# Optimization experiments

Hardware: AMD Instinct MI355X
Metric: run time of the kernel (lower is better)

The kernel has to match this reference:

```python
import jax, jax.numpy as jnp
import numpy as np

HEADS = 4
NEG_SLOPE = 0.2  # PyG GATConv default


def gat_layer(x, src, dst, W, a_src, a_dst, b):
    """PyG-style GATConv: gather -> per-edge attention -> segment softmax -> scatter.
    x: [N, Fin], W: [Fin, H*C], a_src/a_dst: [H, C], b: [H*C]."""
    N = x.shape[0]
    h = (x @ W).reshape(N, HEADS, -1)                      # [N, H, C]
    alpha_s = jnp.einsum('nhc,hc->nh', h, a_src)           # [N, H]
    alpha_d = jnp.einsum('nhc,hc->nh', h, a_dst)           # [N, H]
    e = jax.nn.leaky_relu(alpha_s[src] + alpha_d[dst], NEG_SLOPE)  # [E, H]
    # segment softmax over incoming edges of each destination node
    m = jax.ops.segment_max(e, dst, num_segments=N)
    m = jnp.where(jnp.isfinite(m), m, 0.0)
    ex = jnp.exp(e - m[dst])
    denom = jax.ops.segment_sum(ex, dst, num_segments=N)
    alpha = ex / (denom[dst] + 1e-16)                      # [E, H]
    msg = h[src] * alpha[:, :, None]                       # [E, H, C]
    out = jax.ops.segment_sum(msg, dst, num_segments=N)    # [N, H, C]
    return out.reshape(N, -1) + b


def setup_inputs() -> dict:
    key = jax.random.key(0)
    ks = jax.random.split(key, 10)
    N, E, FIN, HID, OUT = 50000, 800000, 128, 128, 128
    hd1, hd2 = HID // HEADS, OUT // HEADS
    x = jax.random.normal(ks[0], (N, FIN), dtype=jnp.float32)
    edge_index = jax.random.randint(ks[1], (2, E), 0, N, dtype=jnp.int32)
    s1 = 1.0 / np.sqrt(FIN)
    s2 = 1.0 / np.sqrt(HID)
    return {
        'x_sub': x,
        'edge_index_sub': edge_index,
        'W1': jax.random.normal(ks[2], (FIN, HEADS * hd1), dtype=jnp.float32) * s1,
        'a_src1': jax.random.normal(ks[3], (HEADS, hd1), dtype=jnp.float32) * 0.1,
        'a_dst1': jax.random.normal(ks[4], (HEADS, hd1), dtype=jnp.float32) * 0.1,
        'b1': jnp.zeros((HEADS * hd1,), dtype=jnp.float32),
        'W2': jax.random.normal(ks[5], (HID, HEADS * hd2), dtype=jnp.float32) * s2,
        'a_src2': jax.random.normal(ks[6], (HEADS, hd2), dtype=jnp.float32) * 0.1,
        'a_dst2': jax.random.normal(ks[7], (HEADS, hd2), dtype=jnp.float32) * 0.1,
        'b2': jnp.zeros((HEADS * hd2,), dtype=jnp.float32),
    }


def reference(x_sub, edge_index_sub, W1, a_src1, a_dst1, b1, W2, a_src2, a_dst2, b2):
    N = x_sub.shape[0]
    # PyG GATConv default add_self_loops=True
    loops = jnp.arange(N, dtype=edge_index_sub.dtype)
    src = jnp.concatenate([edge_index_sub[0], loops])
    dst = jnp.concatenate([edge_index_sub[1], loops])
    h = gat_layer(x_sub, src, dst, W1, a_src1, a_dst1, b1)
    h = jax.nn.relu(h)  # dropout p=0.5 is identity in eval mode
    out = gat_layer(h, src, dst, W2, a_src2, a_dst2, b2)
    return out
```

## Files before the change

### kernel.cpp

```cpp
#include <hip/hip_runtime.h>
#include <hip/hip_fp16.h>

#define HEADS 4
#define F 128
#define NEG_SLOPE 0.2f

#define NB 256
#define NPB 196
#define BE 5888
#define CAPS 6144

#define LDP 136
#define SMEM_BYTES 52224

typedef _Float16 f16x8 __attribute__((ext_vector_type(8)));
typedef _Float16 f16x4 __attribute__((ext_vector_type(4)));
typedef float f32x4 __attribute__((ext_vector_type(4)));

__device__ __forceinline__ float lrelu(float v) { return v > 0.f ? v : NEG_SLOPE * v; }

__global__ __launch_bounds__(256) void k_wcvt_hist(const float* __restrict__ W1,
                                                   const float* __restrict__ W2,
                                                   _Float16* __restrict__ Wt1,
                                                   _Float16* __restrict__ Wt2,
                                                   const int* __restrict__ dst,
                                                   int* __restrict__ histSlots,
                                                   int E, int gB) {
    __shared__ _Float16 l[128][LDP];
    __shared__ int hh[NB];
    int t = threadIdx.x;
    int bx = blockIdx.x;
    if (bx >= gB) {
        const float* W = (bx - gB) ? W2 : W1;
        _Float16* Wt = (bx - gB) ? Wt2 : Wt1;
        for (int i = t; i < 4096; i += 256) {
            int k = i >> 5, n4 = (i & 31) << 2;
            float4 v = ((const float4*)W)[i];
            l[n4][k]     = (_Float16)v.x;
            l[n4 + 1][k] = (_Float16)v.y;
            l[n4 + 2][k] = (_Float16)v.z;
            l[n4 + 3][k] = (_Float16)v.w;
        }
        __syncthreads();
        for (int i = t; i < 2048; i += 256) {
            int n = i >> 4, c8 = (i & 15) << 3;
            *(f16x8*)(Wt + n * 128 + c8) = *(const f16x8*)(&l[n][c8]);
        }
        return;
    }
    hh[t] = 0;
    __syncthreads();
    int base = bx * BE;
    int end = min(base + BE, E);
    for (int i = base + t; i < end; i += 256) atomicAdd(&hh[dst[i] / NPB], 1);
    __syncthreads();
    histSlots[bx * NB + t] = hh[t];
}

__global__ __launch_bounds__(NB) void k_bscan(const int* __restrict__ histSlots, int gB,
                                              int* __restrict__ bucketCnt,
                                              int* __restrict__ edgeStart,
                                              int* __restrict__ srcStart,
                                              int* __restrict__ bucketCursor,
                                              int* __restrict__ rowstart, int N) {
    __shared__ int ws1[4], ws2[4];
    int t = threadIdx.x, lane = t & 63, w = t >> 6;
    int c = 0;
    for (int i = 0; i < gB; ++i) c += histSlots[i * NB + t];
    bucketCnt[t] = c;
    int nIn = N - t * NPB; nIn = nIn < 0 ? 0 : (nIn > NPB ? NPB : nIn);
    int s = c + nIn;
    int x1 = c, x2 = s;
#pragma unroll
    for (int off = 1; off < 64; off <<= 1) {
        int a = __shfl_up(x1, off), b = __shfl_up(x2, off);
        if (lane >= off) { x1 += a; x2 += b; }
    }
    if (lane == 63) { ws1[w] = x1; ws2[w] = x2; }
    __syncthreads();
    int o1 = 0, o2 = 0;
    for (int i = 0; i < w; ++i) { o1 += ws1[i]; o2 += ws2[i]; }
    int e1 = o1 + x1 - c;
    int e2 = o2 + x2 - s;
    edgeStart[t] = e1; srcStart[t] = e2; bucketCursor[t] = e1;
    if (t == NB - 1) {
        edgeStart[NB] = e1 + c;
        srcStart[NB] = e2 + s;
        rowstart[N] = e2 + s;
    }
}

__global__ __launch_bounds__(256) void k_scat_gemm(const int* __restrict__ src,
                                                   const int* __restrict__ dst,
                                                   int* __restrict__ bucketCursor,
                                                   uint2* __restrict__ temp, int E, int gB,
                                                   const float* __restrict__ X,
                                                   const _Float16* __restrict__ Wt,
                                                   const float* __restrict__ asrc,
                                                   const float* __restrict__ adst,
                                                   _Float16* __restrict__ Hh,
                                                   float* __restrict__ As,
                                                   float* __restrict__ Ad, int N) {
    __shared__ __align__(16) char smem[SMEM_BYTES];
    int t = threadIdx.x;
    int bx = blockIdx.x;

    if (bx < gB) {
        uint2* se   = (uint2*)smem;
        int* hist   = (int*)(smem + BE * 8);
        int* lofs   = hist + NB;
        int* lcur   = lofs + NB;
        int* gbase  = lcur + NB;
        int* wsum   = gbase + NB;
        hist[t] = 0;
        __syncthreads();
        int base = bx * BE;
        int end = min(base + BE, E);
        for (int i = base + t; i < end; i += 256) atomicAdd(&hist[dst[i] / NPB], 1);
        __syncthreads();
        {
            int lane = t & 63, w = t >> 6;
            int c = hist[t], x = c;
#pragma unroll
            for (int off = 1; off < 64; off <<= 1) {
                int a = __shfl_up(x, off);
                if (lane >= off) x += a;
            }
            if (lane == 63) wsum[w] = x;
            __syncthreads();
            int o = 0;
            for (int i = 0; i < w; ++i) o += wsum[i];
            int ex = o + x - c;
            lofs[t] = ex;
            lcur[t] = ex;
            gbase[t] = c ? atomicAdd(&bucketCursor[t], c) : 0;
        }
        __syncthreads();
        for (int i = base + t; i < end; i += 256) {
            int d = dst[i];
            int b = d / NPB;
            int dl = d - b * NPB;
            int pos = atomicAdd(&lcur[b], 1);
            se[pos] = make_uint2((unsigned)src[i], (unsigned)((b << 8) | dl));
        }
        __syncthreads();
        int tot = end - base;
        for (int i = t; i < tot; i += 256) {
            uint2 e = se[i];
            int b = (int)(e.y >> 8);
            temp[gbase[b] + (i - lofs[b])] = e;
        }
        return;
    }

    _Float16* xs = (_Float16*)smem;
    _Float16* ws = xs + 64 * LDP;
    int row0 = (bx - gB) * 64;

    for (int i = t; i < 128 * 16; i += 256) {
        int rw = i >> 4, c8 = (i & 15) << 3;
        *(f16x8*)(ws + rw * LDP + c8) = *(const f16x8*)(Wt + rw * 128 + c8);
    }
    for (int i = t; i < 64 * 32; i += 256) {
        int r = i >> 5, c4 = (i & 31) << 2;
        int gr = row0 + r;
        float4 v = (gr < N) ? *(const float4*)(X + (size_t)gr * F + c4)
                            : make_float4(0.f, 0.f, 0.f, 0.f);
        f16x4 h4 = {(_Float16)v.x, (_Float16)v.y, (_Float16)v.z, (_Float16)v.w};
        *(f16x4*)(xs + r * LDP + c4) = h4;
    }
    __syncthreads();

    int w = t >> 6, lane = t & 63, q = lane >> 4, r = lane & 15;
    f32x4 acc[8] = {};
    const _Float16* xrow = xs + (w * 16 + r) * LDP;
    const _Float16* wrow = ws + r * LDP;
#pragma unroll
    for (int kk = 0; kk < 4; ++kk) {
        f16x8 bxv = *(const f16x8*)(xrow + kk * 32 + q * 8);
#pragma unroll
        for (int nt = 0; nt < 8; ++nt) {
            f16x8 af = *(const f16x8*)(wrow + nt * 16 * LDP + kk * 32 + q * 8);
            acc[nt] = __builtin_amdgcn_mfma_f32_16x16x32_f16(af, bxv, acc[nt], 0, 0, 0);
        }
    }
    int m = row0 + w * 16 + r;

    float sh[4], dh[4];
#pragma unroll
    for (int h = 0; h < 4; ++h) {
        float s = 0.f, d = 0.f;
#pragma unroll
        for (int k2 = 0; k2 < 2; ++k2) {
            int nt = h * 2 + k2;
            float4 av = ((const float4*)asrc)[nt * 4 + q];
            float4 bv = ((const float4*)adst)[nt * 4 + q];
            s += acc[nt][0] * av.x + acc[nt][1] * av.y + acc[nt][2] * av.z + acc[nt][3] * av.w;
            d += acc[nt][0] * bv.x + acc[nt][1] * bv.y + acc[nt][2] * bv.z + acc[nt][3] * bv.w;
        }
        s += __shfl_xor(s, 16); s += __shfl_xor(s, 32);
        d += __shfl_xor(d, 16); d += __shfl_xor(d, 32);
        sh[h] = s; dh[h] = d;
    }
    if (q == 0 && m < N) {
        ((float4*)As)[m] = make_float4(sh[0], sh[1], sh[2], sh[3]);
        ((float4*)Ad)[m] = make_float4(dh[0], dh[1], dh[2], dh[3]);
    }
    if (m < N) {
        _Float16* hp = Hh + (size_t)m * F + q * 4;
#pragma unroll
        for (int nt = 0; nt < 8; ++nt) {
            f16x4 h4 = {(_Float16)acc[nt][0], (_Float16)acc[nt][1],
                        (_Float16)acc[nt][2], (_Float16)acc[nt][3]};
            *(f16x4*)(hp + nt * 16) = h4;
        }
    }
}

__global__ __launch_bounds__(256) void k_gemm_mfma(const _Float16* __restrict__ Xh,
                                                   const _Float16* __restrict__ Wt,
                                                   const float* __restrict__ asrc,
                                                   const float* __restrict__ adst,
                                                   _Float16* __restrict__ Hh,
                                                   float* __restrict__ As,
                                                   float* __restrict__ Ad, int N) {
    __shared__ _Float16 xs[64 * LDP];
    __shared__ _Float16 ws[128 * LDP];
    int t = threadIdx.x;
    int row0 = blockIdx.x * 64;

    for (int i = t; i < 128 * 16; i += 256) {
        int rw = i >> 4, c8 = (i & 15) << 3;
        *(f16x8*)(ws + rw * LDP + c8) = *(const f16x8*)(Wt + rw * 128 + c8);
    }
    for (int i = t; i < 64 * 16; i += 256) {
        int r = i >> 4, c8 = (i & 15) << 3;
        int gr = row0 + r;
        f16x8 v = {0, 0, 0, 0, 0, 0, 0, 0};
        if (gr < N) v = *(const f16x8*)(Xh + (size_t)gr * F + c8);
        *(f16x8*)(xs + r * LDP + c8) = v;
    }
    __syncthreads();

    int w = t >> 6, lane = t & 63, q = lane >> 4, r = lane & 15;
    f32x4 acc[8] = {};
    const _Float16* xrow = xs + (w * 16 + r) * LDP;
    const _Float16* wrow = ws + r * LDP;
#pragma unroll
    for (int kk = 0; kk < 4; ++kk) {
        f16x8 bxv = *(const f16x8*)(xrow + kk * 32 + q * 8);
#pragma unroll
        for (int nt = 0; nt < 8; ++nt) {
            f16x8 af = *(const f16x8*)(wrow + nt * 16 * LDP + kk * 32 + q * 8);
            acc[nt] = __builtin_amdgcn_mfma_f32_16x16x32_f16(af, bxv, acc[nt], 0, 0, 0);
        }
    }
    int m = row0 + w * 16 + r;

    float sh[4], dh[4];
#pragma unroll
    for (int h = 0; h < 4; ++h) {
        float s = 0.f, d = 0.f;
#pragma unroll
        for (int k2 = 0; k2 < 2; ++k2) {
            int nt = h * 2 + k2;
            float4 av = ((const float4*)asrc)[nt * 4 + q];
            float4 bv = ((const float4*)adst)[nt * 4 + q];
            s += acc[nt][0] * av.x + acc[nt][1] * av.y + acc[nt][2] * av.z + acc[nt][3] * av.w;
            d += acc[nt][0] * bv.x + acc[nt][1] * bv.y + acc[nt][2] * bv.z + acc[nt][3] * bv.w;
        }
        s += __shfl_xor(s, 16); s += __shfl_xor(s, 32);
        d += __shfl_xor(d, 16); d += __shfl_xor(d, 32);
        sh[h] = s; dh[h] = d;
    }
    if (q == 0 && m < N) {
        ((float4*)As)[m] = make_float4(sh[0], sh[1], sh[2], sh[3]);
        ((float4*)Ad)[m] = make_float4(dh[0], dh[1], dh[2], dh[3]);
    }
    if (m < N) {
        _Float16* hp = Hh + (size_t)m * F + q * 4;
#pragma unroll
        for (int nt = 0; nt < 8; ++nt) {
            f16x4 h4 = {(_Float16)acc[nt][0], (_Float16)acc[nt][1],
                        (_Float16)acc[nt][2], (_Float16)acc[nt][3]};
            *(f16x4*)(hp + nt * 16) = h4;
        }
    }
}

__global__ __launch_bounds__(256) void k_bsort(const uint2* __restrict__ temp,
                                               const int* __restrict__ edgeStart,
                                               const int* __restrict__ srcStart,
                                               const int* __restrict__ bucketCnt,
                                               int* __restrict__ rowstart,
                                               int* __restrict__ srcs, int N) {
    __shared__ int cnt[NPB];
    __shared__ int scanE[NPB];
    __shared__ int outS[CAPS];
    __shared__ int wsum[4];
    int b = blockIdx.x, t = threadIdx.x;
    int eBase = edgeStart[b], eCnt = bucketCnt[b];
    int sBase = srcStart[b];
    int nIn = N - b * NPB; nIn = nIn < 0 ? 0 : (nIn > NPB ? NPB : nIn);
    for (int i = t; i < NPB; i += 256) cnt[i] = 1;
    __syncthreads();
    for (int i = t; i < eCnt; i += 256) {
        uint2 e = temp[eBase + i];
        atomicAdd(&cnt[e.y & 0xFF], 1);
    }
    __syncthreads();
    {
        int lane = t & 63, w = t >> 6;
        int c = (t < nIn) ? cnt[t] : 0;
        int x = c;
#pragma unroll
        for (int off = 1; off < 64; off <<= 1) {
            int a = __shfl_up(x, off);
            if (lane >= off) x += a;
        }
        if (lane == 63) wsum[w] = x;
        __syncthreads();
        int o = 0;
        for (int i = 0; i < w; ++i) o += wsum[i];
        if (t < nIn) scanE[t] = o + x - c;
    }
    __syncthreads();
    if (t < nIn) {
        int s0 = scanE[t];
        outS[s0] = b * NPB + t;
        cnt[t] = s0 + 1;
        rowstart[b * NPB + t] = sBase + s0;
    }
    __syncthreads();
    for (int i = t; i < eCnt; i += 256) {
        uint2 e = temp[eBase + i];
        int pos = atomicAdd(&cnt[e.y & 0xFF], 1);
        if (pos < CAPS) outS[pos] = (int)e.x;
    }
    __syncthreads();
    int tot = eCnt + nIn;
    for (int i = t; i < tot; i += 256) srcs[sBase + i] = outS[i];
}

template <bool RELU, bool OUTH>
__global__ __launch_bounds__(256) void k_aggr(const int* __restrict__ rowstart,
                                              const int* __restrict__ srcs,
                                              const float* __restrict__ As,
                                              const float* __restrict__ Ad,
                                              const _Float16* __restrict__ Hh,
                                              const float* __restrict__ bias,
                                              void* __restrict__ Ov, int N) {
    __shared__ float exs_s[4][256];
    int wid = threadIdx.x >> 6;
    float* exs = exs_s[wid];
    int w = (blockIdx.x << 2) + wid;
    int lane = threadIdx.x & 63;
    if (w >= N) return;
    int d = w;
    int b0 = rowstart[d], b1 = rowstart[d + 1];
    int g = lane >> 4, l16 = lane & 15;
    int h = l16 >> 2;
    float4 ad4 = ((const float4*)Ad)[d];
    float den = 0.f;
    float acc[8] = {};

    for (int base = b0; base < b1; base += 64) {
        int cnt = min(64, b1 - base);
        int myv = (lane < cnt) ? srcs[base + lane] : 0;
        if (lane < cnt) {
            float4 a4 = ((const float4*)As)[myv];
            float4 e;
            e.x = __expf(lrelu(a4.x + ad4.x));
            e.y = __expf(lrelu(a4.y + ad4.y));
            e.z = __expf(lrelu(a4.z + ad4.z));
            e.w = __expf(lrelu(a4.w + ad4.w));
            ((float4*)exs)[lane] = e;
        }
        int j = 0;
        for (; j + 8 <= cnt; j += 8) {
            int s0 = __shfl(myv, j + g);
            int s1 = __shfl(myv, j + 4 + g);
            float4 q0 = *(const float4*)(Hh + (size_t)s0 * F + 8 * l16);
            float4 q1 = *(const float4*)(Hh + (size_t)s1 * F + 8 * l16);
            float e0 = exs[(j + g) * 4 + h];
            float e1 = exs[(j + 4 + g) * 4 + h];
            den += e0 + e1;
            const __half2* p0 = (const __half2*)&q0;
            const __half2* p1 = (const __half2*)&q1;
#pragma unroll
            for (int u = 0; u < 4; ++u) {
                float2 f0 = __half22float2(p0[u]);
                float2 f1 = __half22float2(p1[u]);
                acc[2 * u]     += e0 * f0.x + e1 * f1.x;
                acc[2 * u + 1] += e0 * f0.y + e1 * f1.y;
            }
        }
        for (; j < cnt; j += 4) {
            int idx = j + g;
            bool ok = idx < cnt;
            int idxc = ok ? idx : (cnt - 1);
            int s0 = __shfl(myv, idxc);
            float e0 = ok ? exs[idx * 4 + h] : 0.f;
            float4 q0 = *(const float4*)(Hh + (size_t)s0 * F + 8 * l16);
            den += e0;
            const __half2* p0 = (const __half2*)&q0;
#pragma unroll
            for (int u = 0; u < 4; ++u) {
                float2 f0 = __half22float2(p0[u]);
                acc[2 * u]     += e0 * f0.x;
                acc[2 * u + 1] += e0 * f0.y;
            }
        }
    }
#pragma unroll
    for (int i = 0; i < 8; ++i) {
        acc[i] += __shfl_xor(acc[i], 16);
        acc[i] += __shfl_xor(acc[i], 32);
    }
    den += __shfl_xor(den, 16);
    den += __shfl_xor(den, 32);
    float inv = 1.f / (den + 1e-16f);

    if (g == 0) {
        float4 bv0 = ((const float4*)bias)[2 * l16];
        float4 bv1 = ((const float4*)bias)[2 * l16 + 1];
        float o[8];
        o[0] = acc[0] * inv + bv0.x; o[1] = acc[1] * inv + bv0.y;
        o[2] = acc[2] * inv + bv0.z; o[3] = acc[3] * inv + bv0.w;
        o[4] = acc[4] * inv + bv1.x; o[5] = acc[5] * inv + bv1.y;
        o[6] = acc[6] * inv + bv1.z; o[7] = acc[7] * inv + bv1.w;
        if (RELU) {
#pragma unroll
            for (int i = 0; i < 8; ++i) o[i] = fmaxf(o[i], 0.f);
        }
        if (OUTH) {
            f16x8 p;
#pragma unroll
            for (int i = 0; i < 8; ++i) p[i] = (_Float16)o[i];
            *(f16x8*)((_Float16*)Ov + (size_t)d * F + 8 * l16) = p;
        } else {
            float* op = (float*)Ov + (size_t)d * F + 8 * l16;
            *(float4*)op = make_float4(o[0], o[1], o[2], o[3]);
            *(float4*)(op + 4) = make_float4(o[4], o[5], o[6], o[7]);
        }
    }
}

extern "C" void kernel_launch(void* const* d_in, const int* in_sizes, int n_in,
                              void* d_out, int out_size, void* d_ws, size_t ws_size,
                              hipStream_t stream) {
    const float* x   = (const float*)d_in[0];
    const int*   ei  = (const int*)d_in[1];
    const float* W1  = (const float*)d_in[2];
    const float* as1 = (const float*)d_in[3];
    const float* ad1 = (const float*)d_in[4];
    const float* b1  = (const float*)d_in[5];
    const float* W2  = (const float*)d_in[6];
    const float* as2 = (const float*)d_in[7];
    const float* ad2 = (const float*)d_in[8];
    const float* b2  = (const float*)d_in[9];

    int N = in_sizes[0] / F;
    int E = in_sizes[1] / 2;
    const int* src = ei;
    const int* dst = ei + E;

    int gB = (E + BE - 1) / BE;
    int gG = (N + 63) / 64;
    int gW = (N + 3) / 4;

    char* base = (char*)d_ws;
    size_t off = 0;
    _Float16* Hh  = (_Float16*)(base + off); off += (size_t)N * F * 2;
    _Float16* O1h = (_Float16*)(base + off); off += (size_t)N * F * 2;
    float* As  = (float*)(base + off);  off += (size_t)N * HEADS * 4;
    float* Ad  = (float*)(base + off);  off += (size_t)N * HEADS * 4;
    int* rowstart = (int*)(base + off); off += (size_t)(N + 1) * 4;
    off = (off + 15) & ~(size_t)15;
    int* srcs = (int*)(base + off);     off += (size_t)(E + N) * 4;
    off = (off + 15) & ~(size_t)15;
    uint2* temp = (uint2*)(base + off); off += (size_t)E * 8;
    int* bucketCnt   = (int*)(base + off); off += NB * 4;
    int* edgeStart   = (int*)(base + off); off += (NB + 1) * 4;
    int* srcStart    = (int*)(base + off); off += (NB + 1) * 4;
    int* bucketCursor= (int*)(base + off); off += NB * 4;
    off = (off + 15) & ~(size_t)15;
    _Float16* Wt1 = (_Float16*)(base + off); off += 128 * 128 * 2;
    _Float16* Wt2 = (_Float16*)(base + off); off += 128 * 128 * 2;
    off = (off + 15) & ~(size_t)15;
    int* histSlots = (int*)(base + off); off += (size_t)gB * NB * 4;

    dim3 blk(256);

    k_wcvt_hist<<<gB + 2, blk, 0, stream>>>(W1, W2, Wt1, Wt2, dst, histSlots, E, gB);
    k_bscan<<<1, NB, 0, stream>>>(histSlots, gB, bucketCnt, edgeStart, srcStart,
                                  bucketCursor, rowstart, N);
    k_scat_gemm<<<gB + gG, blk, 0, stream>>>(src, dst, bucketCursor, temp, E, gB,
                                             x, Wt1, as1, ad1, Hh, As, Ad, N);
    k_bsort<<<NB, blk, 0, stream>>>(temp, edgeStart, srcStart, bucketCnt, rowstart, srcs, N);

    k_aggr<true, true><<<gW, blk, 0, stream>>>(rowstart, srcs, As, Ad, Hh, b1, O1h, N);

    k_gemm_mfma<<<gG, blk, 0, stream>>>(O1h, Wt2, as2, ad2, Hh, As, Ad, N);
    k_aggr<false, false><<<gW, blk, 0, stream>>>(rowstart, srcs, As, Ad, Hh, b2, d_out, N);
}
```

Baseline: 158.7 us.

## Reuse per-block histograms as scatter offsets, drop recount and LDS staging

The bucket scan kernel now converts each block's histogram slots into exclusive global write offsets. The scatter blocks then start their per-bucket cursors from those offsets instead of re-histogramming dst, scanning, and atomically reserving space on a global cursor. Edges are written straight to temp from the atomic cursor, with no staging in LDS and no second copy pass. This removes a full extra read of dst and several barriers, but gives up the coalesced staged write. The block size BE is also raised to 8192, which cuts the histogram slot count and the length of the serial per-bucket loop in the single-block scan.

```diff
diff --git a/kernel.cpp b/kernel.cpp
--- a/kernel.cpp
+++ b/kernel.cpp
@@ -7,7 +7,7 @@
 
 #define NB 256
 #define NPB 196
-#define BE 5888
+#define BE 8192
 #define CAPS 6144
 
 #define LDP 136
@@ -57,11 +57,10 @@
     histSlots[bx * NB + t] = hh[t];
 }
 
-__global__ __launch_bounds__(NB) void k_bscan(const int* __restrict__ histSlots, int gB,
+__global__ __launch_bounds__(NB) void k_bscan(int* __restrict__ histSlots, int gB,
                                               int* __restrict__ bucketCnt,
                                               int* __restrict__ edgeStart,
                                               int* __restrict__ srcStart,
-                                              int* __restrict__ bucketCursor,
                                               int* __restrict__ rowstart, int N) {
     __shared__ int ws1[4], ws2[4];
     int t = threadIdx.x, lane = t & 63, w = t >> 6;
@@ -82,17 +81,23 @@
     for (int i = 0; i < w; ++i) { o1 += ws1[i]; o2 += ws2[i]; }
     int e1 = o1 + x1 - c;
     int e2 = o2 + x2 - s;
-    edgeStart[t] = e1; srcStart[t] = e2; bucketCursor[t] = e1;
+    edgeStart[t] = e1; srcStart[t] = e2;
     if (t == NB - 1) {
         edgeStart[NB] = e1 + c;
         srcStart[NB] = e2 + s;
         rowstart[N] = e2 + s;
     }
+    int run = e1;
+    for (int i = 0; i < gB; ++i) {
+        int v = histSlots[i * NB + t];
+        histSlots[i * NB + t] = run;
+        run += v;
+    }
 }
 
 __global__ __launch_bounds__(256) void k_scat_gemm(const int* __restrict__ src,
                                                    const int* __restrict__ dst,
-                                                   int* __restrict__ bucketCursor,
+                                                   const int* __restrict__ blockBase,
                                                    uint2* __restrict__ temp, int E, int gB,
                                                    const float* __restrict__ X,
                                                    const _Float16* __restrict__ Wt,
@@ -106,49 +111,17 @@
     int bx = blockIdx.x;
 
     if (bx < gB) {
-        uint2* se   = (uint2*)smem;
-        int* hist   = (int*)(smem + BE * 8);
-        int* lofs   = hist + NB;
-        int* lcur   = lofs + NB;
-        int* gbase  = lcur + NB;
-        int* wsum   = gbase + NB;
-        hist[t] = 0;
+        int* lcur = (int*)smem;
+        lcur[t] = blockBase[bx * NB + t];
         __syncthreads();
         int base = bx * BE;
         int end = min(base + BE, E);
-        for (int i = base + t; i < end; i += 256) atomicAdd(&hist[dst[i] / NPB], 1);
-        __syncthreads();
-        {
-            int lane = t & 63, w = t >> 6;
-            int c = hist[t], x = c;
-#pragma unroll
-            for (int off = 1; off < 64; off <<= 1) {
-                int a = __shfl_up(x, off);
-                if (lane >= off) x += a;
-            }
-            if (lane == 63) wsum[w] = x;
-            __syncthreads();
-            int o = 0;
-            for (int i = 0; i < w; ++i) o += wsum[i];
-            int ex = o + x - c;
-            lofs[t] = ex;
-            lcur[t] = ex;
-            gbase[t] = c ? atomicAdd(&bucketCursor[t], c) : 0;
-        }
-        __syncthreads();
         for (int i = base + t; i < end; i += 256) {
             int d = dst[i];
             int b = d / NPB;
             int dl = d - b * NPB;
             int pos = atomicAdd(&lcur[b], 1);
-            se[pos] = make_uint2((unsigned)src[i], (unsigned)((b << 8) | dl));
-        }
-        __syncthreads();
-        int tot = end - base;
-        for (int i = t; i < tot; i += 256) {
-            uint2 e = se[i];
-            int b = (int)(e.y >> 8);
-            temp[gbase[b] + (i - lofs[b])] = e;
+            temp[pos] = make_uint2((unsigned)src[i], (unsigned)((b << 8) | dl));
         }
         return;
     }
@@ -483,7 +456,6 @@
     int* bucketCnt   = (int*)(base + off); off += NB * 4;
     int* edgeStart   = (int*)(base + off); off += (NB + 1) * 4;
     int* srcStart    = (int*)(base + off); off += (NB + 1) * 4;
-    int* bucketCursor= (int*)(base + off); off += NB * 4;
     off = (off + 15) & ~(size_t)15;
     _Float16* Wt1 = (_Float16*)(base + off); off += 128 * 128 * 2;
     _Float16* Wt2 = (_Float16*)(base + off); off += 128 * 128 * 2;
@@ -494,8 +466,8 @@
 
     k_wcvt_hist<<<gB + 2, blk, 0, stream>>>(W1, W2, Wt1, Wt2, dst, histSlots, E, gB);
     k_bscan<<<1, NB, 0, stream>>>(histSlots, gB, bucketCnt, edgeStart, srcStart,
-                                  bucketCursor, rowstart, N);
-    k_scat_gemm<<<gB + gG, blk, 0, stream>>>(src, dst, bucketCursor, temp, E, gB,
+                                  rowstart, N);
+    k_scat_gemm<<<gB + gG, blk, 0, stream>>>(src, dst, histSlots, temp, E, gB,
                                              x, Wt1, as1, ad1, Hh, As, Ad, N);
     k_bsort<<<NB, blk, 0, stream>>>(temp, edgeStart, srcStart, bucketCnt, rowstart, srcs, N);
 
```

Result: slower. 162.0 us (+2.1%).
